# Kernel tuning notes

Hardware: AMD Instinct MI355X
Metric: run time of the kernel (lower is better)

Reference implementation:

```python
import jax, jax.numpy as jnp
import numpy as np

WINDOW_SIZE = 512
CAUSAL = True

def _sliding_window_mask(seq_len, window_size, causal):
    i = jnp.arange(seq_len)[:, None]
    j = jnp.arange(seq_len)[None, :]
    mask = (j >= i - window_size + 1) & (j <= i)
    if causal:
        mask = mask & (j <= i)
    return mask  # [S, S] bool, True = attend


def setup_inputs() -> dict:
    key = jax.random.key(0)
    k1, k2, k3 = jax.random.split(key, 3)
    B, S, D = 16, 4096, 64
    q = jax.random.normal(k1, (B, S, D), dtype=jnp.float32)
    k = jax.random.normal(k2, (B, S, D), dtype=jnp.float32)
    v = jax.random.normal(k3, (B, S, D), dtype=jnp.float32)
    return {"q": q, "k": k, "v": v}


def reference(q, k, v):
    B, S, D = q.shape
    scale = D ** -0.5
    mask = _sliding_window_mask(S, WINDOW_SIZE, CAUSAL)  # [S, S]
    scores = jnp.einsum("bqd,bkd->bqk", q, k) * scale    # [B, S, S]
    mask_value = -jnp.finfo(scores.dtype).max
    scores = jnp.where(mask[None, :, :], scores, mask_value)
    attn = jax.nn.softmax(scores, axis=-1)
    out = jnp.einsum("bqk,bkd->bqd", attn, v)            # [B, S, D]
    return out
```

## Files before the change

### kernel.cpp

```cpp
#include <hip/hip_runtime.h>

#define BATCH 16
#define SEQ   4096
#define DIM   64
#define WIN   512

constexpr int BM = 64;
constexpr int BN = 64;
constexpr int NTHREADS = 256;
constexpr int KS = DIM + 8;
constexpr int VS = BN + 4;
constexpr int OS = DIM + 4;
constexpr int KBYTES   = BN * KS * 2;
constexpr int VBYTES   = DIM * VS * 2;
constexpr int BUFBYTES = KBYTES + VBYTES;
constexpr int SMEMBYTES = 2 * BUFBYTES;

constexpr float QSCALE  = 0.125f * 1.44269504088896340736f;
constexpr float MASKVAL = -3.0e38f;
constexpr float DEFER_THR = 8.0f;

typedef _Float16 f16x2 __attribute__((ext_vector_type(2)));
typedef _Float16 f16x4 __attribute__((ext_vector_type(4)));
typedef _Float16 f16x8 __attribute__((ext_vector_type(8)));
typedef float    f32x4 __attribute__((ext_vector_type(4)));

__device__ __forceinline__ f16x2 pk2(float a, float b) {
    return __builtin_bit_cast(f16x2, __builtin_amdgcn_cvt_pkrtz(a, b));
}

struct Pref {
    float4 k0, k1, k2, k3;
    float4 v0, v1, v2, v3;
};

__device__ __forceinline__ void load_tile(Pref& p, const float* __restrict__ kb,
                                          const float* __restrict__ vb,
                                          int kbase, int row4, int c4) {
    const size_t g = (size_t)(kbase + row4) * DIM + c4;
    p.k0 = *(const float4*)&kb[g + 0 * DIM];
    p.k1 = *(const float4*)&kb[g + 1 * DIM];
    p.k2 = *(const float4*)&kb[g + 2 * DIM];
    p.k3 = *(const float4*)&kb[g + 3 * DIM];
    p.v0 = *(const float4*)&vb[g + 0 * DIM];
    p.v1 = *(const float4*)&vb[g + 1 * DIM];
    p.v2 = *(const float4*)&vb[g + 2 * DIM];
    p.v3 = *(const float4*)&vb[g + 3 * DIM];
}

__device__ __forceinline__ void stage_tile(char* __restrict__ buf, const Pref& p,
                                           int row4, int c4) {
    _Float16* Ksh = (_Float16*)buf;
    _Float16* Vsh = (_Float16*)(buf + KBYTES);
    union { f16x4 v; f16x2 h[2]; } u;
    u.h[0] = pk2(p.k0.x, p.k0.y); u.h[1] = pk2(p.k0.z, p.k0.w);
    *(f16x4*)&Ksh[(row4 + 0) * KS + c4] = u.v;
    u.h[0] = pk2(p.k1.x, p.k1.y); u.h[1] = pk2(p.k1.z, p.k1.w);
    *(f16x4*)&Ksh[(row4 + 1) * KS + c4] = u.v;
    u.h[0] = pk2(p.k2.x, p.k2.y); u.h[1] = pk2(p.k2.z, p.k2.w);
    *(f16x4*)&Ksh[(row4 + 2) * KS + c4] = u.v;
    u.h[0] = pk2(p.k3.x, p.k3.y); u.h[1] = pk2(p.k3.z, p.k3.w);
    *(f16x4*)&Ksh[(row4 + 3) * KS + c4] = u.v;
    const float* f0 = (const float*)&p.v0;
    const float* f1 = (const float*)&p.v1;
    const float* f2 = (const float*)&p.v2;
    const float* f3 = (const float*)&p.v3;
    #pragma unroll
    for (int j = 0; j < 4; ++j) {
        u.h[0] = pk2(f0[j], f1[j]);
        u.h[1] = pk2(f2[j], f3[j]);
        *(f16x4*)&Vsh[(c4 + j) * VS + row4] = u.v;
    }
}

__global__ __launch_bounds__(NTHREADS, 4)
void swa_kernel(const float* __restrict__ qg, const float* __restrict__ kg,
                const float* __restrict__ vg, float* __restrict__ outg) {
    __shared__ __align__(16) char smem[SMEMBYTES];
    float* Osh = (float*)smem;

    const int tid  = threadIdx.x;
    const int lane = tid & 63;
    const int wave = tid >> 6;
    const int lr   = lane & 15;
    const int quad = lane >> 4;

    static_assert(SEQ / BM == 64 && BATCH == 16, "swizzle assumes 1024 blocks");
    const int lin    = blockIdx.x + (SEQ / BM) * blockIdx.y;
    const int xcd    = lin & 7;
    const int slot   = lin >> 3;
    const int member = slot & 7;
    const int gchunk = (slot >> 3) * 8 + xcd;
    const int b      = gchunk >> 3;
    const int qblk   = (gchunk & 7) * 8 + member;

    const int qrow0 = qblk * BM;
    const int wr0   = qrow0 + wave * 16;
    const int q     = wr0 + lr;

    const float* qb = qg + (size_t)b * SEQ * DIM;
    const float* kb = kg + (size_t)b * SEQ * DIM;
    const float* vb = vg + (size_t)b * SEQ * DIM;
    float*       ob = outg + (size_t)b * SEQ * DIM;

    const int row4 = (tid >> 4) * 4;
    const int c4   = (tid & 15) * 4;

    const float* qp = qb + (size_t)q * DIM + quad * 8;
    const float4 a0 = *(const float4*)(qp + 0);
    const float4 a1 = *(const float4*)(qp + 4);
    const float4 a2 = *(const float4*)(qp + 32);
    const float4 a3 = *(const float4*)(qp + 36);
    union { f16x8 v; f16x2 h[4]; } uq0, uq1;
    uq0.h[0] = pk2(a0.x * QSCALE, a0.y * QSCALE);
    uq0.h[1] = pk2(a0.z * QSCALE, a0.w * QSCALE);
    uq0.h[2] = pk2(a1.x * QSCALE, a1.y * QSCALE);
    uq0.h[3] = pk2(a1.z * QSCALE, a1.w * QSCALE);
    uq1.h[0] = pk2(a2.x * QSCALE, a2.y * QSCALE);
    uq1.h[1] = pk2(a2.z * QSCALE, a2.w * QSCALE);
    uq1.h[2] = pk2(a3.x * QSCALE, a3.y * QSCALE);
    uq1.h[3] = pk2(a3.z * QSCALE, a3.w * QSCALE);
    const f16x8 qf0 = uq0.v, qf1 = uq1.v;

    f32x4 o[4];
    #pragma unroll
    for (int mi = 0; mi < 4; ++mi) o[mi] = (f32x4){0.f, 0.f, 0.f, 0.f};
    float m_run = -1e30f, l_run = 0.f;

    const int t0 = (qrow0 > (WIN - 1)) ? (qrow0 - (WIN - 1)) >> 6 : 0;
    const int t1 = (qrow0 + BM - 1) >> 6;

    Pref pf;
    load_tile(pf, kb, vb, t0 * BN, row4, c4);
    stage_tile(smem, pf, row4, c4);
    __syncthreads();

    for (int t = t0; t <= t1; ++t) {
        const int cb = (t - t0) & 1;
        const _Float16* Kc = (const _Float16*)(smem + cb * BUFBYTES);
        const _Float16* Vc = (const _Float16*)(smem + cb * BUFBYTES + KBYTES);
        const bool have_next = (t < t1);

        if (have_next) load_tile(pf, kb, vb, (t + 1) * BN, row4, c4);
        __builtin_amdgcn_sched_barrier(0);

        const int kbase = t * BN;
        const int u    = (wr0 - kbase) >> 4;
        const int mtlo = (u - 32 > 0) ? u - 32 : 0;
        const int mthi = (u < 3) ? u : 3;

        f32x4 sc[4];
        #pragma unroll
        for (int mt = 0; mt < 4; ++mt) {
            if (mt >= mtlo && mt <= mthi) {
                const f16x8 kf0 = *(const f16x8*)&Kc[(mt * 16 + lr) * KS + quad * 8];
                const f16x8 kf1 = *(const f16x8*)&Kc[(mt * 16 + lr) * KS + 32 + quad * 8];
                f32x4 s = (f32x4){0.f, 0.f, 0.f, 0.f};
                s = __builtin_amdgcn_mfma_f32_16x16x32_f16(kf0, qf0, s, 0, 0, 0);
                s = __builtin_amdgcn_mfma_f32_16x16x32_f16(kf1, qf1, s, 0, 0, 0);
                sc[mt] = s;
            }
        }

        const bool edge = (kbase + mtlo * 16 < wr0 + 15 - (WIN - 1)) ||
                          (kbase + mthi * 16 + 15 > wr0);
        if (edge) {
            #pragma unroll
            for (int mt = 0; mt < 4; ++mt) {
                if (mt >= mtlo && mt <= mthi) {
                    #pragma unroll
                    for (int r = 0; r < 4; ++r) {
                        const int key = kbase + mt * 16 + quad * 4 + r;
                        sc[mt][r] = ((unsigned)(q - key) < (unsigned)WIN) ? sc[mt][r] : MASKVAL;
                    }
                }
            }
        }

        float pm = MASKVAL;
        #pragma unroll
        for (int mt = 0; mt < 4; ++mt) {
            if (mt >= mtlo && mt <= mthi) {
                pm = fmaxf(pm, fmaxf(fmaxf(sc[mt][0], sc[mt][1]),
                                     fmaxf(sc[mt][2], sc[mt][3])));
            }
        }
        pm = fmaxf(pm, __shfl_xor(pm, 16));
        pm = fmaxf(pm, __shfl_xor(pm, 32));

        if (__any(pm > m_run + DEFER_THR)) {
            const float mn    = fmaxf(m_run, pm);
            const float alpha = exp2f(m_run - mn);
            m_run = mn;
            l_run *= alpha;
            #pragma unroll
            for (int mi = 0; mi < 4; ++mi) o[mi] = o[mi] * alpha;
        }

        f16x4 pb[4];
        float ls = 0.f;
        #pragma unroll
        for (int nt = 0; nt < 4; ++nt) {
            if (nt >= mtlo && nt <= mthi) {
                const float p0 = exp2f(sc[nt][0] - m_run);
                const float p1 = exp2f(sc[nt][1] - m_run);
                const float p2 = exp2f(sc[nt][2] - m_run);
                const float p3 = exp2f(sc[nt][3] - m_run);
                ls += (p0 + p1) + (p2 + p3);
                union { f16x4 v; f16x2 h[2]; } up;
                up.h[0] = pk2(p0, p1);
                up.h[1] = pk2(p2, p3);
                pb[nt] = up.v;
            }
        }
        l_run += ls;

        #pragma unroll
        for (int nt = 0; nt < 4; ++nt) {
            if (nt >= mtlo && nt <= mthi) {
                #pragma unroll
                for (int mi = 0; mi < 4; ++mi) {
                    const f16x4 vf = *(const f16x4*)&Vc[(mi * 16 + lr) * VS + nt * 16 + quad * 4];
                    o[mi] = __builtin_amdgcn_mfma_f32_16x16x16f16(vf, pb[nt], o[mi], 0, 0, 0);
                }
            }
        }

        if (have_next) stage_tile(smem + (cb ^ 1) * BUFBYTES, pf, row4, c4);
        __syncthreads();
    }

    l_run += __shfl_xor(l_run, 16);
    l_run += __shfl_xor(l_run, 32);
    const float inv = 1.0f / l_run;

    float* Ow = Osh + wave * 16 * OS;
    #pragma unroll
    for (int mi = 0; mi < 4; ++mi) {
        float4 st;
        st.x = o[mi][0] * inv; st.y = o[mi][1] * inv;
        st.z = o[mi][2] * inv; st.w = o[mi][3] * inv;
        *(float4*)&Ow[lr * OS + mi * 16 + quad * 4] = st;
    }
    #pragma unroll
    for (int j = 0; j < 4; ++j) {
        const int qq = quad + 4 * j;
        const int d4 = lr * 4;
        const float4 vst = *(const float4*)&Ow[qq * OS + d4];
        *(float4*)&ob[(size_t)(wr0 + qq) * DIM + d4] = vst;
    }
}

extern "C" void kernel_launch(void* const* d_in, const int* in_sizes, int n_in,
                              void* d_out, int out_size, void* d_ws, size_t ws_size,
                              hipStream_t stream) {
    (void)in_sizes; (void)n_in; (void)out_size; (void)d_ws; (void)ws_size;
    const float* q = (const float*)d_in[0];
    const float* k = (const float*)d_in[1];
    const float* v = (const float*)d_in[2];
    float* out = (float*)d_out;
    dim3 grid(SEQ / BM, BATCH);
    swa_kernel<<<grid, dim3(NTHREADS), 0, stream>>>(q, k, v, out);
}
```

Baseline: 116.1 us.

## Precast K and transpose V to fp16 in a prep kernel, drop LDS staging

Adds a prep kernel that converts K to fp16 and writes V transposed as fp16 into workspace. The main kernel then reads MFMA fragments straight from global memory (L2/cache) with no shared-memory double buffering or block syncs, and each wave iterates only over its own key range. This removes the per-block fp32 loads, conversion and LDS staging, at the cost of an extra kernel launch and a full pass over K/V. It also relies on cache hits for uncoalesced fragment loads and on the workspace being large enough.

```diff
diff --git a/kernel.cpp b/kernel.cpp
--- a/kernel.cpp
+++ b/kernel.cpp
@@ -8,13 +8,6 @@
 constexpr int BM = 64;
 constexpr int BN = 64;
 constexpr int NTHREADS = 256;
-constexpr int KS = DIM + 8;
-constexpr int VS = BN + 4;
-constexpr int OS = DIM + 4;
-constexpr int KBYTES   = BN * KS * 2;
-constexpr int VBYTES   = DIM * VS * 2;
-constexpr int BUFBYTES = KBYTES + VBYTES;
-constexpr int SMEMBYTES = 2 * BUFBYTES;
 
 constexpr float QSCALE  = 0.125f * 1.44269504088896340736f;
 constexpr float MASKVAL = -3.0e38f;
@@ -29,56 +22,53 @@
     return __builtin_bit_cast(f16x2, __builtin_amdgcn_cvt_pkrtz(a, b));
 }
 
-struct Pref {
-    float4 k0, k1, k2, k3;
-    float4 v0, v1, v2, v3;
-};
-
-__device__ __forceinline__ void load_tile(Pref& p, const float* __restrict__ kb,
-                                          const float* __restrict__ vb,
-                                          int kbase, int row4, int c4) {
-    const size_t g = (size_t)(kbase + row4) * DIM + c4;
-    p.k0 = *(const float4*)&kb[g + 0 * DIM];
-    p.k1 = *(const float4*)&kb[g + 1 * DIM];
-    p.k2 = *(const float4*)&kb[g + 2 * DIM];
-    p.k3 = *(const float4*)&kb[g + 3 * DIM];
-    p.v0 = *(const float4*)&vb[g + 0 * DIM];
-    p.v1 = *(const float4*)&vb[g + 1 * DIM];
-    p.v2 = *(const float4*)&vb[g + 2 * DIM];
-    p.v3 = *(const float4*)&vb[g + 3 * DIM];
-}
-
-__device__ __forceinline__ void stage_tile(char* __restrict__ buf, const Pref& p,
-                                           int row4, int c4) {
-    _Float16* Ksh = (_Float16*)buf;
-    _Float16* Vsh = (_Float16*)(buf + KBYTES);
-    union { f16x4 v; f16x2 h[2]; } u;
-    u.h[0] = pk2(p.k0.x, p.k0.y); u.h[1] = pk2(p.k0.z, p.k0.w);
-    *(f16x4*)&Ksh[(row4 + 0) * KS + c4] = u.v;
-    u.h[0] = pk2(p.k1.x, p.k1.y); u.h[1] = pk2(p.k1.z, p.k1.w);
-    *(f16x4*)&Ksh[(row4 + 1) * KS + c4] = u.v;
-    u.h[0] = pk2(p.k2.x, p.k2.y); u.h[1] = pk2(p.k2.z, p.k2.w);
-    *(f16x4*)&Ksh[(row4 + 2) * KS + c4] = u.v;
-    u.h[0] = pk2(p.k3.x, p.k3.y); u.h[1] = pk2(p.k3.z, p.k3.w);
-    *(f16x4*)&Ksh[(row4 + 3) * KS + c4] = u.v;
-    const float* f0 = (const float*)&p.v0;
-    const float* f1 = (const float*)&p.v1;
-    const float* f2 = (const float*)&p.v2;
-    const float* f3 = (const float*)&p.v3;
-    #pragma unroll
-    for (int j = 0; j < 4; ++j) {
-        u.h[0] = pk2(f0[j], f1[j]);
-        u.h[1] = pk2(f2[j], f3[j]);
-        *(f16x4*)&Vsh[(c4 + j) * VS + row4] = u.v;
-    }
-}
-
+__global__ __launch_bounds__(256)
+void prep_kernel(const float* __restrict__ kg, const float* __restrict__ vg,
+                 _Float16* __restrict__ k16, _Float16* __restrict__ vt16, int do_k) {
+    __shared__ _Float16 tile[64][72];
+    const int t  = threadIdx.x;
+    const int b  = blockIdx.y;
+    const int s0 = blockIdx.x * 64;
+    const int r  = t >> 4;
+    const int c4 = (t & 15) * 4;
+
+    const float* vbp = vg + ((size_t)b * SEQ + s0) * DIM;
+    #pragma unroll
+    for (int i = 0; i < 4; ++i) {
+        const int row = r + i * 16;
+        const float4 v4 = *(const float4*)&vbp[(size_t)row * DIM + c4];
+        union { f16x4 h4; f16x2 h2[2]; } u;
+        u.h2[0] = pk2(v4.x, v4.y); u.h2[1] = pk2(v4.z, v4.w);
+        *(f16x4*)&tile[row][c4] = u.h4;
+    }
+    if (do_k) {
+        const float* kbp = kg + ((size_t)b * SEQ + s0) * DIM;
+        _Float16*    kop = k16 + ((size_t)b * SEQ + s0) * DIM;
+        #pragma unroll
+        for (int i = 0; i < 4; ++i) {
+            const int row = r + i * 16;
+            const float4 v4 = *(const float4*)&kbp[(size_t)row * DIM + c4];
+            union { f16x4 h4; f16x2 h2[2]; } u;
+            u.h2[0] = pk2(v4.x, v4.y); u.h2[1] = pk2(v4.z, v4.w);
+            *(f16x4*)&kop[(size_t)row * DIM + c4] = u.h4;
+        }
+    }
+    __syncthreads();
+    const int d   = t >> 2;
+    const int sc_ = (t & 3) * 16;
+    _Float16* vop = vt16 + ((size_t)b * DIM + d) * SEQ + s0 + sc_;
+    union { f16x8 h8; _Float16 e[8]; } w0, w1;
+    #pragma unroll
+    for (int j = 0; j < 8; ++j) { w0.e[j] = tile[sc_ + j][d]; w1.e[j] = tile[sc_ + 8 + j][d]; }
+    *(f16x8*)&vop[0] = w0.h8;
+    *(f16x8*)&vop[8] = w1.h8;
+}
+
+template<bool K16EN>
 __global__ __launch_bounds__(NTHREADS, 4)
-void swa_kernel(const float* __restrict__ qg, const float* __restrict__ kg,
-                const float* __restrict__ vg, float* __restrict__ outg) {
-    __shared__ __align__(16) char smem[SMEMBYTES];
-    float* Osh = (float*)smem;
-
+void swa_main(const float* __restrict__ qg, const float* __restrict__ kg,
+              float* __restrict__ outg,
+              const _Float16* __restrict__ k16, const _Float16* __restrict__ vt16) {
     const int tid  = threadIdx.x;
     const int lane = tid & 63;
     const int wave = tid >> 6;
@@ -86,7 +76,7 @@
     const int quad = lane >> 4;
 
     static_assert(SEQ / BM == 64 && BATCH == 16, "swizzle assumes 1024 blocks");
-    const int lin    = blockIdx.x + (SEQ / BM) * blockIdx.y;
+    const int lin    = blockIdx.x;
     const int xcd    = lin & 7;
     const int slot   = lin >> 3;
     const int member = slot & 7;
@@ -98,13 +88,11 @@
     const int wr0   = qrow0 + wave * 16;
     const int q     = wr0 + lr;
 
-    const float* qb = qg + (size_t)b * SEQ * DIM;
-    const float* kb = kg + (size_t)b * SEQ * DIM;
-    const float* vb = vg + (size_t)b * SEQ * DIM;
-    float*       ob = outg + (size_t)b * SEQ * DIM;
-
-    const int row4 = (tid >> 4) * 4;
-    const int c4   = (tid & 15) * 4;
+    const float*    qb  = qg  + (size_t)b * SEQ * DIM;
+    const float*    kb  = kg  + (size_t)b * SEQ * DIM;
+    float*          ob  = outg + (size_t)b * SEQ * DIM;
+    const _Float16* kfb = K16EN ? (k16 + (size_t)b * SEQ * DIM) : nullptr;
+    const _Float16* vtb = vt16 + (size_t)b * DIM * SEQ;
 
     const float* qp = qb + (size_t)q * DIM + quad * 8;
     const float4 a0 = *(const float4*)(qp + 0);
@@ -127,34 +115,38 @@
     for (int mi = 0; mi < 4; ++mi) o[mi] = (f32x4){0.f, 0.f, 0.f, 0.f};
     float m_run = -1e30f, l_run = 0.f;
 
-    const int t0 = (qrow0 > (WIN - 1)) ? (qrow0 - (WIN - 1)) >> 6 : 0;
-    const int t1 = (qrow0 + BM - 1) >> 6;
-
-    Pref pf;
-    load_tile(pf, kb, vb, t0 * BN, row4, c4);
-    stage_tile(smem, pf, row4, c4);
-    __syncthreads();
+    const int lo = (wr0 > (WIN - 1)) ? wr0 - (WIN - 1) : 0;
+    const int t0 = lo >> 6;
+    const int t1 = (wr0 + 15) >> 6;
 
     for (int t = t0; t <= t1; ++t) {
-        const int cb = (t - t0) & 1;
-        const _Float16* Kc = (const _Float16*)(smem + cb * BUFBYTES);
-        const _Float16* Vc = (const _Float16*)(smem + cb * BUFBYTES + KBYTES);
-        const bool have_next = (t < t1);
-
-        if (have_next) load_tile(pf, kb, vb, (t + 1) * BN, row4, c4);
-        __builtin_amdgcn_sched_barrier(0);
-
         const int kbase = t * BN;
-        const int u    = (wr0 - kbase) >> 4;
-        const int mtlo = (u - 32 > 0) ? u - 32 : 0;
-        const int mthi = (u < 3) ? u : 3;
+        const int u     = (wr0 - kbase) >> 4;
+        const int mtlo  = (u - 32 > 0) ? u - 32 : 0;
+        const int mthi  = (u < 3) ? u : 3;
 
         f32x4 sc[4];
         #pragma unroll
         for (int mt = 0; mt < 4; ++mt) {
             if (mt >= mtlo && mt <= mthi) {
-                const f16x8 kf0 = *(const f16x8*)&Kc[(mt * 16 + lr) * KS + quad * 8];
-                const f16x8 kf1 = *(const f16x8*)&Kc[(mt * 16 + lr) * KS + 32 + quad * 8];
+                f16x8 kf0, kf1;
+                if constexpr (K16EN) {
+                    const _Float16* kp = kfb + (size_t)(kbase + mt * 16 + lr) * DIM + quad * 8;
+                    kf0 = *(const f16x8*)(kp + 0);
+                    kf1 = *(const f16x8*)(kp + 32);
+                } else {
+                    const float* kp = kb + (size_t)(kbase + mt * 16 + lr) * DIM + quad * 8;
+                    const float4 x0 = *(const float4*)(kp + 0);
+                    const float4 x1 = *(const float4*)(kp + 4);
+                    const float4 x2 = *(const float4*)(kp + 32);
+                    const float4 x3 = *(const float4*)(kp + 36);
+                    union { f16x8 v; f16x2 h[4]; } u0, u1;
+                    u0.h[0] = pk2(x0.x, x0.y); u0.h[1] = pk2(x0.z, x0.w);
+                    u0.h[2] = pk2(x1.x, x1.y); u0.h[3] = pk2(x1.z, x1.w);
+                    u1.h[0] = pk2(x2.x, x2.y); u1.h[1] = pk2(x2.z, x2.w);
+                    u1.h[2] = pk2(x3.x, x3.y); u1.h[3] = pk2(x3.z, x3.w);
+                    kf0 = u0.v; kf1 = u1.v;
+                }
                 f32x4 s = (f32x4){0.f, 0.f, 0.f, 0.f};
                 s = __builtin_amdgcn_mfma_f32_16x16x32_f16(kf0, qf0, s, 0, 0, 0);
                 s = __builtin_amdgcn_mfma_f32_16x16x32_f16(kf1, qf1, s, 0, 0, 0);
@@ -220,45 +212,43 @@
             if (nt >= mtlo && nt <= mthi) {
                 #pragma unroll
                 for (int mi = 0; mi < 4; ++mi) {
-                    const f16x4 vf = *(const f16x4*)&Vc[(mi * 16 + lr) * VS + nt * 16 + quad * 4];
+                    const f16x4 vf = *(const f16x4*)&vtb[(size_t)(mi * 16 + lr) * SEQ
+                                                          + kbase + nt * 16 + quad * 4];
                     o[mi] = __builtin_amdgcn_mfma_f32_16x16x16f16(vf, pb[nt], o[mi], 0, 0, 0);
                 }
             }
         }
-
-        if (have_next) stage_tile(smem + (cb ^ 1) * BUFBYTES, pf, row4, c4);
-        __syncthreads();
     }
 
     l_run += __shfl_xor(l_run, 16);
     l_run += __shfl_xor(l_run, 32);
     const float inv = 1.0f / l_run;
-
-    float* Ow = Osh + wave * 16 * OS;
     #pragma unroll
     for (int mi = 0; mi < 4; ++mi) {
         float4 st;
         st.x = o[mi][0] * inv; st.y = o[mi][1] * inv;
         st.z = o[mi][2] * inv; st.w = o[mi][3] * inv;
-        *(float4*)&Ow[lr * OS + mi * 16 + quad * 4] = st;
-    }
-    #pragma unroll
-    for (int j = 0; j < 4; ++j) {
-        const int qq = quad + 4 * j;
-        const int d4 = lr * 4;
-        const float4 vst = *(const float4*)&Ow[qq * OS + d4];
-        *(float4*)&ob[(size_t)(wr0 + qq) * DIM + d4] = vst;
+        *(float4*)&ob[(size_t)q * DIM + mi * 16 + quad * 4] = st;
     }
 }
 
 extern "C" void kernel_launch(void* const* d_in, const int* in_sizes, int n_in,
                               void* d_out, int out_size, void* d_ws, size_t ws_size,
                               hipStream_t stream) {
-    (void)in_sizes; (void)n_in; (void)out_size; (void)d_ws; (void)ws_size;
+    (void)in_sizes; (void)n_in; (void)out_size;
     const float* q = (const float*)d_in[0];
     const float* k = (const float*)d_in[1];
     const float* v = (const float*)d_in[2];
     float* out = (float*)d_out;
-    dim3 grid(SEQ / BM, BATCH);
-    swa_kernel<<<grid, dim3(NTHREADS), 0, stream>>>(q, k, v, out);
-}
+
+    const size_t KVB = (size_t)BATCH * SEQ * DIM * sizeof(_Float16);
+    _Float16* vt16 = (_Float16*)d_ws;
+    const bool k16en = ws_size >= 2 * KVB;
+    _Float16* k16 = k16en ? (_Float16*)((char*)d_ws + KVB) : nullptr;
+
+    prep_kernel<<<dim3(SEQ / 64, BATCH), dim3(256), 0, stream>>>(k, v, k16, vt16, (int)k16en);
+    if (k16en)
+        swa_main<true ><<<dim3(BATCH * SEQ / BM), dim3(NTHREADS), 0, stream>>>(q, k, out, k16, vt16);
+    else
+        swa_main<false><<<dim3(BATCH * SEQ / BM), dim3(NTHREADS), 0, stream>>>(q, k, out, k16, vt16);
+}
```

New measurement: 183.8 us. 1.58x slower.

## Double query rows per wave to reuse K/V fragments, panelize V in LDS

Applied to the files above, without the earlier changes.

Raises the query block to 128 rows so each wave handles two 16-row query tiles, reusing every K and V fragment read from LDS across two MFMA streams. The V tile is rearranged into four 16-key panels with a smaller padded stride, MFMA phases are wrapped in s_setprio, and the grid swizzle is adapted to 512 blocks. The aim is to halve K/V global loads and LDS traffic per query row. The costs are doubled accumulator and score registers (launch bounds drop to 2 blocks per SIMD), half as many blocks, and extra wasted tiles at the causal and window edges.

```diff
diff --git a/kernel.cpp b/kernel.cpp
--- a/kernel.cpp
+++ b/kernel.cpp
@@ -5,14 +5,15 @@
 #define DIM   64
 #define WIN   512
 
-constexpr int BM = 64;
+constexpr int BM = 128;
 constexpr int BN = 64;
 constexpr int NTHREADS = 256;
-constexpr int KS = DIM + 8;
-constexpr int VS = BN + 4;
-constexpr int OS = DIM + 4;
+constexpr int KS  = DIM + 8;
+constexpr int VSP = 20;
+constexpr int OS  = DIM + 4;
 constexpr int KBYTES   = BN * KS * 2;
-constexpr int VBYTES   = DIM * VS * 2;
+constexpr int VPANEL   = DIM * VSP * 2;
+constexpr int VBYTES   = 4 * VPANEL;
 constexpr int BUFBYTES = KBYTES + VBYTES;
 constexpr int SMEMBYTES = 2 * BUFBYTES;
 
@@ -61,6 +62,7 @@
     *(f16x4*)&Ksh[(row4 + 2) * KS + c4] = u.v;
     u.h[0] = pk2(p.k3.x, p.k3.y); u.h[1] = pk2(p.k3.z, p.k3.w);
     *(f16x4*)&Ksh[(row4 + 3) * KS + c4] = u.v;
+    const int pbase = (row4 >> 4) * (DIM * VSP) + (row4 & 15);
     const float* f0 = (const float*)&p.v0;
     const float* f1 = (const float*)&p.v1;
     const float* f2 = (const float*)&p.v2;
@@ -69,11 +71,11 @@
     for (int j = 0; j < 4; ++j) {
         u.h[0] = pk2(f0[j], f1[j]);
         u.h[1] = pk2(f2[j], f3[j]);
-        *(f16x4*)&Vsh[(c4 + j) * VS + row4] = u.v;
-    }
-}
-
-__global__ __launch_bounds__(NTHREADS, 4)
+        *(f16x4*)&Vsh[pbase + (c4 + j) * VSP] = u.v;
+    }
+}
+
+__global__ __launch_bounds__(NTHREADS, 2)
 void swa_kernel(const float* __restrict__ qg, const float* __restrict__ kg,
                 const float* __restrict__ vg, float* __restrict__ outg) {
     __shared__ __align__(16) char smem[SMEMBYTES];
@@ -85,18 +87,19 @@
     const int lr   = lane & 15;
     const int quad = lane >> 4;
 
-    static_assert(SEQ / BM == 64 && BATCH == 16, "swizzle assumes 1024 blocks");
+    static_assert(SEQ / BM == 32 && BATCH == 16, "swizzle assumes 512 blocks");
     const int lin    = blockIdx.x + (SEQ / BM) * blockIdx.y;
     const int xcd    = lin & 7;
     const int slot   = lin >> 3;
-    const int member = slot & 7;
-    const int gchunk = (slot >> 3) * 8 + xcd;
+    const int member = slot & 3;
+    const int gchunk = (slot >> 2) * 8 + xcd;
     const int b      = gchunk >> 3;
-    const int qblk   = (gchunk & 7) * 8 + member;
+    const int qblk   = (gchunk & 7) * 4 + member;
 
     const int qrow0 = qblk * BM;
-    const int wr0   = qrow0 + wave * 16;
-    const int q     = wr0 + lr;
+    const int wr0   = qrow0 + wave * 32;
+    const int q0    = wr0 + lr;
+    const int q1    = wr0 + 16 + lr;
 
     const float* qb = qg + (size_t)b * SEQ * DIM;
     const float* kb = kg + (size_t)b * SEQ * DIM;
@@ -106,26 +109,33 @@
     const int row4 = (tid >> 4) * 4;
     const int c4   = (tid & 15) * 4;
 
-    const float* qp = qb + (size_t)q * DIM + quad * 8;
-    const float4 a0 = *(const float4*)(qp + 0);
-    const float4 a1 = *(const float4*)(qp + 4);
-    const float4 a2 = *(const float4*)(qp + 32);
-    const float4 a3 = *(const float4*)(qp + 36);
-    union { f16x8 v; f16x2 h[4]; } uq0, uq1;
-    uq0.h[0] = pk2(a0.x * QSCALE, a0.y * QSCALE);
-    uq0.h[1] = pk2(a0.z * QSCALE, a0.w * QSCALE);
-    uq0.h[2] = pk2(a1.x * QSCALE, a1.y * QSCALE);
-    uq0.h[3] = pk2(a1.z * QSCALE, a1.w * QSCALE);
-    uq1.h[0] = pk2(a2.x * QSCALE, a2.y * QSCALE);
-    uq1.h[1] = pk2(a2.z * QSCALE, a2.w * QSCALE);
-    uq1.h[2] = pk2(a3.x * QSCALE, a3.y * QSCALE);
-    uq1.h[3] = pk2(a3.z * QSCALE, a3.w * QSCALE);
-    const f16x8 qf0 = uq0.v, qf1 = uq1.v;
-
-    f32x4 o[4];
-    #pragma unroll
-    for (int mi = 0; mi < 4; ++mi) o[mi] = (f32x4){0.f, 0.f, 0.f, 0.f};
-    float m_run = -1e30f, l_run = 0.f;
+    f16x8 qf0[2], qf1[2];
+    #pragma unroll
+    for (int qt = 0; qt < 2; ++qt) {
+        const float* qp = qb + (size_t)(wr0 + qt * 16 + lr) * DIM + quad * 8;
+        const float4 a0 = *(const float4*)(qp + 0);
+        const float4 a1 = *(const float4*)(qp + 4);
+        const float4 a2 = *(const float4*)(qp + 32);
+        const float4 a3 = *(const float4*)(qp + 36);
+        union { f16x8 v; f16x2 h[4]; } u0, u1;
+        u0.h[0] = pk2(a0.x * QSCALE, a0.y * QSCALE);
+        u0.h[1] = pk2(a0.z * QSCALE, a0.w * QSCALE);
+        u0.h[2] = pk2(a1.x * QSCALE, a1.y * QSCALE);
+        u0.h[3] = pk2(a1.z * QSCALE, a1.w * QSCALE);
+        u1.h[0] = pk2(a2.x * QSCALE, a2.y * QSCALE);
+        u1.h[1] = pk2(a2.z * QSCALE, a2.w * QSCALE);
+        u1.h[2] = pk2(a3.x * QSCALE, a3.y * QSCALE);
+        u1.h[3] = pk2(a3.z * QSCALE, a3.w * QSCALE);
+        qf0[qt] = u0.v; qf1[qt] = u1.v;
+    }
+
+    f32x4 o[2][4];
+    #pragma unroll
+    for (int qt = 0; qt < 2; ++qt)
+        #pragma unroll
+        for (int mi = 0; mi < 4; ++mi) o[qt][mi] = (f32x4){0.f, 0.f, 0.f, 0.f};
+    float m_run[2] = {-1e30f, -1e30f};
+    float l_run[2] = {0.f, 0.f};
 
     const int t0 = (qrow0 > (WIN - 1)) ? (qrow0 - (WIN - 1)) >> 6 : 0;
     const int t1 = (qrow0 + BM - 1) >> 6;
@@ -147,107 +157,125 @@
         const int kbase = t * BN;
         const int u    = (wr0 - kbase) >> 4;
         const int mtlo = (u - 32 > 0) ? u - 32 : 0;
-        const int mthi = (u < 3) ? u : 3;
-
-        f32x4 sc[4];
-        #pragma unroll
-        for (int mt = 0; mt < 4; ++mt) {
-            if (mt >= mtlo && mt <= mthi) {
-                const f16x8 kf0 = *(const f16x8*)&Kc[(mt * 16 + lr) * KS + quad * 8];
-                const f16x8 kf1 = *(const f16x8*)&Kc[(mt * 16 + lr) * KS + 32 + quad * 8];
-                f32x4 s = (f32x4){0.f, 0.f, 0.f, 0.f};
-                s = __builtin_amdgcn_mfma_f32_16x16x32_f16(kf0, qf0, s, 0, 0, 0);
-                s = __builtin_amdgcn_mfma_f32_16x16x32_f16(kf1, qf1, s, 0, 0, 0);
-                sc[mt] = s;
-            }
-        }
-
-        const bool edge = (kbase + mtlo * 16 < wr0 + 15 - (WIN - 1)) ||
-                          (kbase + mthi * 16 + 15 > wr0);
-        if (edge) {
+        const int mthi = (u + 1 < 3) ? u + 1 : 3;
+
+        if (mtlo <= mthi) {
+            f32x4 sc[2][4];
+            __builtin_amdgcn_s_setprio(1);
             #pragma unroll
             for (int mt = 0; mt < 4; ++mt) {
                 if (mt >= mtlo && mt <= mthi) {
+                    const f16x8 kf0 = *(const f16x8*)&Kc[(mt * 16 + lr) * KS + quad * 8];
+                    const f16x8 kf1 = *(const f16x8*)&Kc[(mt * 16 + lr) * KS + 32 + quad * 8];
                     #pragma unroll
-                    for (int r = 0; r < 4; ++r) {
-                        const int key = kbase + mt * 16 + quad * 4 + r;
-                        sc[mt][r] = ((unsigned)(q - key) < (unsigned)WIN) ? sc[mt][r] : MASKVAL;
-                    }
-                }
-            }
-        }
-
-        float pm = MASKVAL;
-        #pragma unroll
-        for (int mt = 0; mt < 4; ++mt) {
-            if (mt >= mtlo && mt <= mthi) {
-                pm = fmaxf(pm, fmaxf(fmaxf(sc[mt][0], sc[mt][1]),
-                                     fmaxf(sc[mt][2], sc[mt][3])));
-            }
-        }
-        pm = fmaxf(pm, __shfl_xor(pm, 16));
-        pm = fmaxf(pm, __shfl_xor(pm, 32));
-
-        if (__any(pm > m_run + DEFER_THR)) {
-            const float mn    = fmaxf(m_run, pm);
-            const float alpha = exp2f(m_run - mn);
-            m_run = mn;
-            l_run *= alpha;
+                    for (int qt = 0; qt < 2; ++qt) {
+                        f32x4 s = (f32x4){0.f, 0.f, 0.f, 0.f};
+                        s = __builtin_amdgcn_mfma_f32_16x16x32_f16(kf0, qf0[qt], s, 0, 0, 0);
+                        s = __builtin_amdgcn_mfma_f32_16x16x32_f16(kf1, qf1[qt], s, 0, 0, 0);
+                        sc[qt][mt] = s;
+                    }
+                }
+            }
+            __builtin_amdgcn_s_setprio(0);
+
+            const bool edge = ((wr0 + 31) - (kbase + mtlo * 16) >= WIN) ||
+                              ((kbase + mthi * 16 + 15) > wr0);
+            if (edge) {
+                #pragma unroll
+                for (int mt = 0; mt < 4; ++mt) {
+                    if (mt >= mtlo && mt <= mthi) {
+                        #pragma unroll
+                        for (int r = 0; r < 4; ++r) {
+                            const int key = kbase + mt * 16 + quad * 4 + r;
+                            sc[0][mt][r] = ((unsigned)(q0 - key) < (unsigned)WIN) ? sc[0][mt][r] : MASKVAL;
+                            sc[1][mt][r] = ((unsigned)(q1 - key) < (unsigned)WIN) ? sc[1][mt][r] : MASKVAL;
+                        }
+                    }
+                }
+            }
+
+            f16x4 pb[2][4];
             #pragma unroll
-            for (int mi = 0; mi < 4; ++mi) o[mi] = o[mi] * alpha;
-        }
-
-        f16x4 pb[4];
-        float ls = 0.f;
-        #pragma unroll
-        for (int nt = 0; nt < 4; ++nt) {
-            if (nt >= mtlo && nt <= mthi) {
-                const float p0 = exp2f(sc[nt][0] - m_run);
-                const float p1 = exp2f(sc[nt][1] - m_run);
-                const float p2 = exp2f(sc[nt][2] - m_run);
-                const float p3 = exp2f(sc[nt][3] - m_run);
-                ls += (p0 + p1) + (p2 + p3);
-                union { f16x4 v; f16x2 h[2]; } up;
-                up.h[0] = pk2(p0, p1);
-                up.h[1] = pk2(p2, p3);
-                pb[nt] = up.v;
-            }
-        }
-        l_run += ls;
-
-        #pragma unroll
-        for (int nt = 0; nt < 4; ++nt) {
-            if (nt >= mtlo && nt <= mthi) {
+            for (int qt = 0; qt < 2; ++qt) {
+                float pm = MASKVAL;
                 #pragma unroll
-                for (int mi = 0; mi < 4; ++mi) {
-                    const f16x4 vf = *(const f16x4*)&Vc[(mi * 16 + lr) * VS + nt * 16 + quad * 4];
-                    o[mi] = __builtin_amdgcn_mfma_f32_16x16x16f16(vf, pb[nt], o[mi], 0, 0, 0);
-                }
-            }
+                for (int mt = 0; mt < 4; ++mt) {
+                    if (mt >= mtlo && mt <= mthi) {
+                        pm = fmaxf(pm, fmaxf(fmaxf(sc[qt][mt][0], sc[qt][mt][1]),
+                                             fmaxf(sc[qt][mt][2], sc[qt][mt][3])));
+                    }
+                }
+                pm = fmaxf(pm, __shfl_xor(pm, 16));
+                pm = fmaxf(pm, __shfl_xor(pm, 32));
+
+                if (__any(pm > m_run[qt] + DEFER_THR)) {
+                    const float mn    = fmaxf(m_run[qt], pm);
+                    const float alpha = exp2f(m_run[qt] - mn);
+                    m_run[qt] = mn;
+                    l_run[qt] *= alpha;
+                    #pragma unroll
+                    for (int mi = 0; mi < 4; ++mi) o[qt][mi] = o[qt][mi] * alpha;
+                }
+
+                float ls = 0.f;
+                #pragma unroll
+                for (int nt = 0; nt < 4; ++nt) {
+                    if (nt >= mtlo && nt <= mthi) {
+                        const float p0 = exp2f(sc[qt][nt][0] - m_run[qt]);
+                        const float p1 = exp2f(sc[qt][nt][1] - m_run[qt]);
+                        const float p2 = exp2f(sc[qt][nt][2] - m_run[qt]);
+                        const float p3 = exp2f(sc[qt][nt][3] - m_run[qt]);
+                        ls += (p0 + p1) + (p2 + p3);
+                        union { f16x4 v; f16x2 h[2]; } up;
+                        up.h[0] = pk2(p0, p1);
+                        up.h[1] = pk2(p2, p3);
+                        pb[qt][nt] = up.v;
+                    }
+                }
+                l_run[qt] += ls;
+            }
+
+            __builtin_amdgcn_s_setprio(1);
+            #pragma unroll
+            for (int nt = 0; nt < 4; ++nt) {
+                if (nt >= mtlo && nt <= mthi) {
+                    #pragma unroll
+                    for (int mi = 0; mi < 4; ++mi) {
+                        const f16x4 vf = *(const f16x4*)&Vc[nt * (DIM * VSP)
+                                             + (mi * 16 + lr) * VSP + quad * 4];
+                        o[0][mi] = __builtin_amdgcn_mfma_f32_16x16x16f16(vf, pb[0][nt], o[0][mi], 0, 0, 0);
+                        o[1][mi] = __builtin_amdgcn_mfma_f32_16x16x16f16(vf, pb[1][nt], o[1][mi], 0, 0, 0);
+                    }
+                }
+            }
+            __builtin_amdgcn_s_setprio(0);
         }
 
         if (have_next) stage_tile(smem + (cb ^ 1) * BUFBYTES, pf, row4, c4);
         __syncthreads();
     }
 
-    l_run += __shfl_xor(l_run, 16);
-    l_run += __shfl_xor(l_run, 32);
-    const float inv = 1.0f / l_run;
-
-    float* Ow = Osh + wave * 16 * OS;
-    #pragma unroll
-    for (int mi = 0; mi < 4; ++mi) {
-        float4 st;
-        st.x = o[mi][0] * inv; st.y = o[mi][1] * inv;
-        st.z = o[mi][2] * inv; st.w = o[mi][3] * inv;
-        *(float4*)&Ow[lr * OS + mi * 16 + quad * 4] = st;
-    }
-    #pragma unroll
-    for (int j = 0; j < 4; ++j) {
-        const int qq = quad + 4 * j;
-        const int d4 = lr * 4;
-        const float4 vst = *(const float4*)&Ow[qq * OS + d4];
-        *(float4*)&ob[(size_t)(wr0 + qq) * DIM + d4] = vst;
+    #pragma unroll
+    for (int qt = 0; qt < 2; ++qt) {
+        float l = l_run[qt];
+        l += __shfl_xor(l, 16);
+        l += __shfl_xor(l, 32);
+        const float inv = 1.0f / l;
+        float* Ow = Osh + (wave * 32 + qt * 16) * OS;
+        #pragma unroll
+        for (int mi = 0; mi < 4; ++mi) {
+            float4 st;
+            st.x = o[qt][mi][0] * inv; st.y = o[qt][mi][1] * inv;
+            st.z = o[qt][mi][2] * inv; st.w = o[qt][mi][3] * inv;
+            *(float4*)&Ow[lr * OS + mi * 16 + quad * 4] = st;
+        }
+        #pragma unroll
+        for (int j = 0; j < 4; ++j) {
+            const int qq = quad + 4 * j;
+            const int d4 = lr * 4;
+            const float4 vst = *(const float4*)&Ow[qq * OS + d4];
+            *(float4*)&ob[(size_t)(wr0 + qt * 16 + qq) * DIM + d4] = vst;
+        }
     }
 }
 
```

Measured after the change: 114.7 us. About the same (-1.2%).
